# Performance work log

Measured on AMD Instinct MI355X. Metric: run time of the kernel, lower is better.

## Reference

```python
import jax, jax.numpy as jnp
import numpy as np

N_NODES = 100000
D = 128
N_EDGES = 800000


def setup_inputs() -> dict:
    key = jax.random.key(0)
    k_feat, k_src, k_dst, k_ws, k_wn = jax.random.split(key, 5)
    scale = 1.0 / np.sqrt(D)
    return {
        "features": jax.random.normal(k_feat, (N_NODES, D), jnp.float32),
        "src": jax.random.randint(k_src, (N_EDGES,), 0, N_NODES, jnp.int32),
        "dst": jax.random.randint(k_dst, (N_EDGES,), 0, N_NODES, jnp.int32),
        "gamma": jnp.ones((D,), jnp.float32),
        "beta": jnp.zeros((D,), jnp.float32),
        "W_self": jax.random.normal(k_ws, (D, D), jnp.float32) * scale,
        "W_neigh": jax.random.normal(k_wn, (D, D), jnp.float32) * scale,
        "b": jnp.zeros((D,), jnp.float32),
    }


def reference(features, src, dst, gamma, beta, W_self, W_neigh, b):
    n = features.shape[0]
    eps = 1e-5
    # BatchNorm1d (training mode: batch stats over the node dim, biased var)
    mean = jnp.mean(features, axis=0)
    var = jnp.mean(jnp.square(features - mean), axis=0)
    h = (features - mean) * jax.lax.rsqrt(var + eps) * gamma + beta  # [N, D]

    # SAGEConv 'mean': gather source feats along edges, mean-reduce per dst node
    msg = h[src]  # [E, D] irregular gather
    agg = jax.ops.segment_sum(msg, dst, num_segments=n)  # [N, D]
    deg = jax.ops.segment_sum(jnp.ones(src.shape, h.dtype), dst, num_segments=n)
    h_neigh = agg / jnp.maximum(deg, 1.0)[:, None]  # zero-degree nodes stay 0

    conv = h @ W_self + h_neigh @ W_neigh + b  # fc_self + fc_neigh + bias
    out = conv + h  # skip connection
    return jax.nn.gelu(out, approximate=False)
```

## Files before the change

### kernel.cpp

```cpp
#include <hip/hip_runtime.h>

#define DD 128
#define NPB_LOG 9
#define NPB 512
#define EPB 1024

typedef __attribute__((ext_vector_type(8))) short short8;
typedef __attribute__((ext_vector_type(4))) float f32x4;

__device__ inline unsigned short f2bf(float f) {
    unsigned u = __float_as_uint(f);
    unsigned r = u + 0x7fffu + ((u >> 16) & 1u);
    return (unsigned short)(r >> 16);
}
__device__ inline float bf2f(unsigned short s) {
    return __uint_as_float(((unsigned)s) << 16);
}

__global__ __launch_bounds__(256) void phase1_k(
    const float4* __restrict__ x, float* __restrict__ stats16, int n,
    const int* __restrict__ dst, int nE, int NCHUNK, int NBUCK,
    const float* __restrict__ Wself, const float* __restrict__ Wneigh,
    unsigned short* __restrict__ Bpre, int* __restrict__ cm) {
    int b = blockIdx.x, tid = threadIdx.x;
    __shared__ float ls[8][256];
    if (b < 16) {
        int q = b * 256 + tid;
        int l = q & 63;
        int kb = ((q >> 9) << 5) + ((l >> 4) << 3);
        int nn = (((q >> 6) & 7) << 4) + (l & 15);
        bool self = (kb < 128);
        const float* Wp = self ? (Wself + (size_t)kb * 128 + nn)
                               : (Wneigh + (size_t)(kb - 128) * 128 + nn);
        unsigned tmp[4];
#pragma unroll
        for (int j = 0; j < 4; ++j) {
            float v0 = Wp[(2 * j) * 128];
            float v1 = Wp[(2 * j + 1) * 128];
            if (self) {
                if (kb + 2 * j == nn) v0 += 1.0f;
                if (kb + 2 * j + 1 == nn) v1 += 1.0f;
            }
            tmp[j] = (unsigned)f2bf(v0) | ((unsigned)f2bf(v1) << 16);
        }
        uint4 w; w.x = tmp[0]; w.y = tmp[1]; w.z = tmp[2]; w.w = tmp[3];
        *(uint4*)(Bpre + (size_t)q * 8) = w;
    } else if (b < 16 + 1024) {
        int bb = b - 16;
        int c4 = tid & 31, sub = tid >> 5;
        float sx = 0.f, sy = 0.f, sz = 0.f, sw = 0.f;
        float qx = 0.f, qy = 0.f, qz = 0.f, qw = 0.f;
        for (int r = bb * 8 + sub; r < n; r += 1024 * 8) {
            float4 v = x[(size_t)r * 32 + c4];
            sx += v.x; sy += v.y; sz += v.z; sw += v.w;
            qx += v.x * v.x; qy += v.y * v.y; qz += v.z * v.z; qw += v.w * v.w;
        }
        ls[sub][c4 * 4 + 0] = sx; ls[sub][c4 * 4 + 1] = sy;
        ls[sub][c4 * 4 + 2] = sz; ls[sub][c4 * 4 + 3] = sw;
        ls[sub][128 + c4 * 4 + 0] = qx; ls[sub][128 + c4 * 4 + 1] = qy;
        ls[sub][128 + c4 * 4 + 2] = qz; ls[sub][128 + c4 * 4 + 3] = qw;
        __syncthreads();
        float t = 0.f;
#pragma unroll
        for (int k = 0; k < 8; ++k) t += ls[k][tid];
        atomicAdd(&stats16[(bb & 15) * 256 + tid], t);
    } else {
        int chunk = b - 1040;
        int* cnt = (int*)ls;
        for (int i = tid; i < NPB; i += 256) cnt[i] = 0;
        __syncthreads();
        int e0 = chunk * EPB;
#pragma unroll
        for (int j = 0; j < 4; ++j) {
            int e = e0 + j * 256 + tid;
            if (e < nE) atomicAdd(&cnt[dst[e] >> NPB_LOG], 1);
        }
        __syncthreads();
        for (int bk = tid; bk < NBUCK; bk += 256)
            cm[(size_t)bk * NCHUNK + chunk] = cnt[bk];
    }
}

__global__ __launch_bounds__(256) void scanA_k(
    const int* __restrict__ v_in, int* __restrict__ bsum, int n) {
    int b = blockIdx.x, t = threadIdx.x;
    int i0 = b * 1024 + t * 4;
    int4 v = {0, 0, 0, 0};
    if (i0 + 3 < n) v = *(const int4*)(v_in + i0);
    else {
        if (i0 < n) v.x = v_in[i0];
        if (i0 + 1 < n) v.y = v_in[i0 + 1];
        if (i0 + 2 < n) v.z = v_in[i0 + 2];
    }
    __shared__ int ls[256];
    ls[t] = v.x + v.y + v.z + v.w;
    __syncthreads();
#pragma unroll
    for (int off = 128; off > 0; off >>= 1) {
        if (t < off) ls[t] += ls[t + off];
        __syncthreads();
    }
    if (t == 0) bsum[b] = ls[0];
}

__global__ __launch_bounds__(256) void scanB_k(
    const int* __restrict__ bsum, int* __restrict__ bpref,
    int* __restrict__ total_out, int nb, int n) {
    __shared__ int ls[256];
    int t = threadIdx.x;
    ls[t] = (t < nb) ? bsum[t] : 0;
    __syncthreads();
#pragma unroll
    for (int off = 1; off < 256; off <<= 1) {
        int x = (t >= off) ? ls[t - off] : 0;
        __syncthreads();
        ls[t] += x;
        __syncthreads();
    }
    if (t < nb) bpref[t] = (t == 0) ? 0 : ls[t - 1];
    if (t == nb - 1) total_out[n] = ls[t];
}

__global__ __launch_bounds__(256) void scanC_k(
    const int* __restrict__ v_in, const int* __restrict__ bpref,
    int* __restrict__ o1, int* __restrict__ o2, int n) {
    int b = blockIdx.x, t = threadIdx.x;
    int i0 = b * 1024 + t * 4;
    int4 v = {0, 0, 0, 0};
    if (i0 + 3 < n) v = *(const int4*)(v_in + i0);
    else {
        if (i0 < n) v.x = v_in[i0];
        if (i0 + 1 < n) v.y = v_in[i0 + 1];
        if (i0 + 2 < n) v.z = v_in[i0 + 2];
    }
    int s = v.x + v.y + v.z + v.w;
    __shared__ int ls[256];
    ls[t] = s;
    __syncthreads();
#pragma unroll
    for (int off = 1; off < 256; off <<= 1) {
        int x = (t >= off) ? ls[t - off] : 0;
        __syncthreads();
        ls[t] += x;
        __syncthreads();
    }
    int run = bpref[b] + ((t == 0) ? 0 : ls[t - 1]);
    int4 o;
    o.x = run; o.y = run + v.x; o.z = o.y + v.y; o.w = o.z + v.z;
    if (i0 + 3 < n) {
        *(int4*)(o1 + i0) = o;
        *(int4*)(o2 + i0) = o;
    } else {
        if (i0 < n) { o1[i0] = o.x; o2[i0] = o.x; }
        if (i0 + 1 < n) { o1[i0 + 1] = o.y; o2[i0 + 1] = o.y; }
        if (i0 + 2 < n) { o1[i0 + 2] = o.z; o2[i0 + 2] = o.z; }
    }
}

__global__ __launch_bounds__(256) void phase2_k(
    const float4* __restrict__ x, const float* __restrict__ stats16,
    const float4* __restrict__ gamma, const float4* __restrict__ beta,
    uint2* __restrict__ hbuf, int n, float inv_n, int nbNorm,
    const int* __restrict__ src, const int* __restrict__ dst,
    const int* __restrict__ cmscan, unsigned* __restrict__ pairs,
    int nE, int NCHUNK, int NBUCK) {
    int b = blockIdx.x, tid = threadIdx.x;
    __shared__ int shr[512];
    if (b < nbNorm) {
        float* fs = (float*)shr;
        float a = 0.f;
#pragma unroll
        for (int sh = 0; sh < 16; ++sh) a += stats16[sh * 256 + tid];
        fs[tid] = a;
        __syncthreads();
        int c4 = tid & 31, sub = tid >> 5;
        int row = b * 8 + sub;
        float4 sm = ((const float4*)fs)[c4], sq = ((const float4*)fs)[32 + c4];
        float4 g = gamma[c4], bt = beta[c4];
        float mx = sm.x * inv_n, my = sm.y * inv_n, mz = sm.z * inv_n, mw = sm.w * inv_n;
        float vx = sq.x * inv_n - mx * mx, vy = sq.y * inv_n - my * my;
        float vz = sq.z * inv_n - mz * mz, vw = sq.w * inv_n - mw * mw;
        float scx = rsqrtf(vx + 1e-5f) * g.x, scy = rsqrtf(vy + 1e-5f) * g.y;
        float scz = rsqrtf(vz + 1e-5f) * g.z, scw = rsqrtf(vw + 1e-5f) * g.w;
        float shx = bt.x - mx * scx, shy = bt.y - my * scy;
        float shz = bt.z - mz * scz, shw = bt.w - mw * scw;
        if (row < n) {
            float4 v = x[(size_t)row * 32 + c4];
            float hx = v.x * scx + shx, hy = v.y * scy + shy;
            float hz = v.z * scz + shz, hw = v.w * scw + shw;
            uint2 o;
            o.x = (unsigned)f2bf(hx) | ((unsigned)f2bf(hy) << 16);
            o.y = (unsigned)f2bf(hz) | ((unsigned)f2bf(hw) << 16);
            hbuf[(size_t)row * 32 + c4] = o;
        }
    } else {
        int chunk = b - nbNorm;
        for (int i = tid; i < NBUCK; i += 256)
            shr[i] = cmscan[(size_t)i * NCHUNK + chunk];
        __syncthreads();
        int e0 = chunk * EPB;
#pragma unroll
        for (int j = 0; j < 4; ++j) {
            int e = e0 + j * 256 + tid;
            if (e < nE) {
                int d = dst[e];
                int p = atomicAdd(&shr[d >> NPB_LOG], 1);
                pairs[p] = ((unsigned)src[e] << NPB_LOG) | (unsigned)(d & (NPB - 1));
            }
        }
    }
}

__global__ __launch_bounds__(256) void sortC_k(
    const unsigned* __restrict__ pairs, const int* __restrict__ cmscan,
    int* __restrict__ offsets, int* __restrict__ csr,
    int n, int nE, int NCHUNK, int NBUCK) {
    int b = blockIdx.x, tid = threadIdx.x;
    int base0 = cmscan[(size_t)b * NCHUNK];
    int end = (b + 1 < NBUCK) ? cmscan[(size_t)(b + 1) * NCHUNK] : nE;
    __shared__ int cnt[NPB];
    __shared__ int cur[NPB];
    __shared__ int ps[256];
    for (int i = tid; i < NPB; i += 256) cnt[i] = 0;
    __syncthreads();
    for (int e = base0 + tid; e < end; e += 256)
        atomicAdd(&cnt[pairs[e] & (NPB - 1)], 1);
    __syncthreads();
    int c0 = cnt[2 * tid], c1 = cnt[2 * tid + 1];
    ps[tid] = c0 + c1;
    __syncthreads();
#pragma unroll
    for (int off = 1; off < 256; off <<= 1) {
        int v = (tid >= off) ? ps[tid - off] : 0;
        __syncthreads();
        ps[tid] += v;
        __syncthreads();
    }
    int ex = base0 + ((tid == 0) ? 0 : ps[tid - 1]);
    cur[2 * tid] = ex;
    cur[2 * tid + 1] = ex + c0;
    int node0 = b * NPB + 2 * tid;
    if (node0 < n) offsets[node0] = ex;
    if (node0 + 1 < n) offsets[node0 + 1] = ex + c0;
    if (b == NBUCK - 1 && tid == 0) offsets[n] = nE;
    __syncthreads();
    for (int e = base0 + tid; e < end; e += 256) {
        unsigned u = pairs[e];
        int p = atomicAdd(&cur[u & (NPB - 1)], 1);
        csr[p] = (int)(u >> NPB_LOG);
    }
}

__global__ __launch_bounds__(256) void pull_k(
    const int* __restrict__ offsets, const int* __restrict__ csr,
    const unsigned* __restrict__ h32, unsigned* __restrict__ hnw, int n) {
    int wid = (blockIdx.x * 256 + threadIdx.x) >> 6;
    int lane = threadIdx.x & 63;
    if (wid >= n) return;
    int b0 = offsets[wid], b1 = offsets[wid + 1];
    float a0 = 0.f, a1 = 0.f;
    int j = b0;
    for (; j + 8 <= b1; j += 8) {
        unsigned u[8];
#pragma unroll
        for (int q = 0; q < 8; ++q) u[q] = h32[(size_t)csr[j + q] * 64 + lane];
#pragma unroll
        for (int q = 0; q < 8; ++q) {
            a0 += bf2f((unsigned short)(u[q] & 0xffff));
            a1 += bf2f((unsigned short)(u[q] >> 16));
        }
    }
    for (; j + 2 <= b1; j += 2) {
        unsigned u0 = h32[(size_t)csr[j] * 64 + lane];
        unsigned u1 = h32[(size_t)csr[j + 1] * 64 + lane];
        a0 += bf2f((unsigned short)(u0 & 0xffff)) + bf2f((unsigned short)(u1 & 0xffff));
        a1 += bf2f((unsigned short)(u0 >> 16)) + bf2f((unsigned short)(u1 >> 16));
    }
    if (j < b1) {
        unsigned u0 = h32[(size_t)csr[j] * 64 + lane];
        a0 += bf2f((unsigned short)(u0 & 0xffff));
        a1 += bf2f((unsigned short)(u0 >> 16));
    }
    float rd = (b1 > b0) ? 1.0f / (float)(b1 - b0) : 0.0f;
    unsigned o = (unsigned)f2bf(a0 * rd) | ((unsigned)f2bf(a1 * rd) << 16);
    hnw[(size_t)wid * 64 + lane] = o;
}

__global__ __launch_bounds__(256, 4) void gemm_k(
    const unsigned short* __restrict__ h, const unsigned short* __restrict__ hn,
    const unsigned short* __restrict__ Bpre, const float* __restrict__ bias,
    float* __restrict__ out, int n) {
    __shared__ unsigned short Bsw[16384];
    int tid = threadIdx.x, wave = tid >> 6, lane = tid & 63;
    int H = blockIdx.x & 1, rb = blockIdx.x >> 1;
#pragma unroll
    for (int i = 0; i < 8; ++i) {
        int g = wave * 8 + i;
        int s = g >> 2, tt = g & 3;
        __builtin_amdgcn_global_load_lds(
            (const __attribute__((address_space(1))) void*)(
                Bpre + ((size_t)((s * 8 + H * 4 + tt) * 64) + lane) * 8),
            (__attribute__((address_space(3))) void*)(Bsw + (size_t)g * 512),
            16, 0, 0);
    }
    __syncthreads();

    int quad = lane >> 4, mrow = lane & 15;
    int r0 = rb * 128 + wave * 32;
    int rA0 = min(r0 + mrow, n - 1);
    int rA1 = min(r0 + 16 + mrow, n - 1);

    f32x4 zero = {0.0f, 0.0f, 0.0f, 0.0f};
    f32x4 acc[2][4];
#pragma unroll
    for (int m = 0; m < 2; ++m)
#pragma unroll
        for (int t = 0; t < 4; ++t) acc[m][t] = zero;

#pragma unroll
    for (int s = 0; s < 8; ++s) {
        int kb = s * 32 + quad * 8;
        short8 a0, a1;
        if (s < 4) {
            a0 = *(const short8*)(h + (size_t)rA0 * 128 + kb);
            a1 = *(const short8*)(h + (size_t)rA1 * 128 + kb);
        } else {
            int kk = kb - 128;
            a0 = *(const short8*)(hn + (size_t)rA0 * 128 + kk);
            a1 = *(const short8*)(hn + (size_t)rA1 * 128 + kk);
        }
#pragma unroll
        for (int tt = 0; tt < 4; ++tt) {
            short8 b = *(const short8*)(Bsw + ((size_t)(s * 4 + tt) * 64 + lane) * 8);
            acc[0][tt] = __builtin_amdgcn_mfma_f32_16x16x32_bf16(a0, b, acc[0][tt], 0, 0, 0);
            acc[1][tt] = __builtin_amdgcn_mfma_f32_16x16x32_bf16(a1, b, acc[1][tt], 0, 0, 0);
        }
    }

    float bi[4];
#pragma unroll
    for (int t = 0; t < 4; ++t) bi[t] = bias[H * 64 + t * 16 + mrow];
#pragma unroll
    for (int m = 0; m < 2; ++m) {
#pragma unroll
        for (int i = 0; i < 4; ++i) {
            int row = r0 + m * 16 + quad * 4 + i;
            if (row < n) {
#pragma unroll
                for (int t = 0; t < 4; ++t) {
                    int col = H * 64 + t * 16 + mrow;
                    float xv = acc[m][t][i] + bi[t];
                    float x2 = xv * xv;
                    float u = 0.7978845608f * xv * (1.0f + 0.044715f * x2);
                    float e = __expf(2.0f * u);
                    float th = 1.0f - 2.0f * __builtin_amdgcn_rcpf(e + 1.0f);
                    out[(size_t)row * 128 + col] = 0.5f * xv * (1.0f + th);
                }
            }
        }
    }
}

extern "C" void kernel_launch(void* const* d_in, const int* in_sizes, int n_in,
                              void* d_out, int out_size, void* d_ws, size_t ws_size,
                              hipStream_t stream) {
    const float* features = (const float*)d_in[0];
    const int* src = (const int*)d_in[1];
    const int* dst = (const int*)d_in[2];
    const float* gamma = (const float*)d_in[3];
    const float* beta = (const float*)d_in[4];
    const float* Wself = (const float*)d_in[5];
    const float* Wneigh = (const float*)d_in[6];
    const float* bias = (const float*)d_in[7];
    int n = in_sizes[0] / DD;
    int nE = in_sizes[1];
    int NCHUNK = (nE + EPB - 1) / EPB;
    int NBUCK = (n + NPB - 1) / NPB;
    int CM = NBUCK * NCHUNK;
    int tilesCM = (CM + 1023) / 1024;
    int nbNorm = (n + 7) / 8;

    auto align1k = [](size_t x) { return (x + 1023) & ~(size_t)1023; };
    char* ws = (char*)d_ws;
    size_t off = 0;
    float* stats16 = (float*)(ws + off);       off += 16384;
    int* cm       = (int*)(ws + off);          off += align1k((size_t)(CM + 1) * 4);
    int* cmscan   = (int*)(ws + off);          off += align1k((size_t)CM * 4);
    int* offsets  = (int*)(ws + off);          off += align1k((size_t)(n + 1) * 4);
    int* csr      = (int*)(ws + off);          off += align1k((size_t)nE * 4);
    unsigned* pairs = (unsigned*)(ws + off);   off += align1k((size_t)nE * 4);
    int* bsum     = (int*)(ws + off);          off += 1024;
    int* bpref    = (int*)(ws + off);          off += 1024;
    unsigned short* Bpre = (unsigned short*)(ws + off); off += 65536;
    unsigned short* hbuf = (unsigned short*)(ws + off); off += (size_t)n * 256;
    unsigned short* hnbuf = (unsigned short*)(ws + off); off += (size_t)n * 256;

    hipMemsetAsync(stats16, 0, 16384, stream);

    phase1_k<<<16 + 1024 + NCHUNK, 256, 0, stream>>>(
        (const float4*)features, stats16, n, dst, nE, NCHUNK, NBUCK,
        Wself, Wneigh, Bpre, cm);
    scanA_k<<<tilesCM, 256, 0, stream>>>(cm, bsum, CM);
    scanB_k<<<1, 256, 0, stream>>>(bsum, bpref, cm, tilesCM, CM);
    scanC_k<<<tilesCM, 256, 0, stream>>>(cm, bpref, cmscan, cmscan, CM);
    phase2_k<<<nbNorm + NCHUNK, 256, 0, stream>>>(
        (const float4*)features, stats16, (const float4*)gamma,
        (const float4*)beta, (uint2*)hbuf, n, 1.0f / (float)n, nbNorm,
        src, dst, cmscan, pairs, nE, NCHUNK, NBUCK);
    sortC_k<<<NBUCK, 256, 0, stream>>>(pairs, cmscan, offsets, csr, n, nE,
                                       NCHUNK, NBUCK);
    pull_k<<<(n * 64 + 255) / 256, 256, 0, stream>>>(
        offsets, csr, (const unsigned*)hbuf, (unsigned*)hnbuf, n);
    gemm_k<<<((n + 127) / 128) * 2, 256, 0, stream>>>(
        hbuf, hnbuf, Bpre, bias, (float*)d_out, n);
}
```

Measured before the change: 226.3 us.

## Gather neighbor features from an FP8 copy and retune bucket and chunk sizes

The normalize pass now also writes an FP8 (e4m3) copy of h alongside the bf16 copy. The neighbor-mean gather reads this copy, which halves the bytes fetched per random edge access in the bandwidth-bound pull stage. Separately, buckets shrink to 256 nodes and edge chunks grow to 2048 edges, which changes the counting-sort grid shapes and simplifies the per-bucket scan to one node per thread. The cost is an extra FP8 write pass and lower aggregation precision, which may push errors past tolerance.

```diff
diff --git a/kernel.cpp b/kernel.cpp
--- a/kernel.cpp
+++ b/kernel.cpp
@@ -1,12 +1,13 @@
 #include <hip/hip_runtime.h>
 
 #define DD 128
-#define NPB_LOG 9
-#define NPB 512
-#define EPB 1024
+#define NPB_LOG 8
+#define NPB 256
+#define EPB 2048
 
 typedef __attribute__((ext_vector_type(8))) short short8;
 typedef __attribute__((ext_vector_type(4))) float f32x4;
+typedef __attribute__((ext_vector_type(2))) float f32x2;
 
 __device__ inline unsigned short f2bf(float f) {
     unsigned u = __float_as_uint(f);
@@ -67,11 +68,11 @@
     } else {
         int chunk = b - 1040;
         int* cnt = (int*)ls;
-        for (int i = tid; i < NPB; i += 256) cnt[i] = 0;
+        for (int i = tid; i < NBUCK; i += 256) cnt[i] = 0;
         __syncthreads();
         int e0 = chunk * EPB;
 #pragma unroll
-        for (int j = 0; j < 4; ++j) {
+        for (int j = 0; j < 8; ++j) {
             int e = e0 + j * 256 + tid;
             if (e < nE) atomicAdd(&cnt[dst[e] >> NPB_LOG], 1);
         }
@@ -160,8 +161,8 @@
 __global__ __launch_bounds__(256) void phase2_k(
     const float4* __restrict__ x, const float* __restrict__ stats16,
     const float4* __restrict__ gamma, const float4* __restrict__ beta,
-    uint2* __restrict__ hbuf, int n, float inv_n, int nbNorm,
-    const int* __restrict__ src, const int* __restrict__ dst,
+    uint2* __restrict__ hbuf, unsigned* __restrict__ h8, int n, float inv_n,
+    int nbNorm, const int* __restrict__ src, const int* __restrict__ dst,
     const int* __restrict__ cmscan, unsigned* __restrict__ pairs,
     int nE, int NCHUNK, int NBUCK) {
     int b = blockIdx.x, tid = threadIdx.x;
@@ -192,6 +193,9 @@
             o.x = (unsigned)f2bf(hx) | ((unsigned)f2bf(hy) << 16);
             o.y = (unsigned)f2bf(hz) | ((unsigned)f2bf(hw) << 16);
             hbuf[(size_t)row * 32 + c4] = o;
+            int p8 = __builtin_amdgcn_cvt_pk_fp8_f32(hx, hy, 0, false);
+            p8 = __builtin_amdgcn_cvt_pk_fp8_f32(hz, hw, p8, true);
+            h8[(size_t)row * 32 + c4] = (unsigned)p8;
         }
     } else {
         int chunk = b - nbNorm;
@@ -200,7 +204,7 @@
         __syncthreads();
         int e0 = chunk * EPB;
 #pragma unroll
-        for (int j = 0; j < 4; ++j) {
+        for (int j = 0; j < 8; ++j) {
             int e = e0 + j * 256 + tid;
             if (e < nE) {
                 int d = dst[e];
@@ -220,14 +224,14 @@
     int end = (b + 1 < NBUCK) ? cmscan[(size_t)(b + 1) * NCHUNK] : nE;
     __shared__ int cnt[NPB];
     __shared__ int cur[NPB];
-    __shared__ int ps[256];
-    for (int i = tid; i < NPB; i += 256) cnt[i] = 0;
+    cnt[tid] = 0;
     __syncthreads();
     for (int e = base0 + tid; e < end; e += 256)
         atomicAdd(&cnt[pairs[e] & (NPB - 1)], 1);
     __syncthreads();
-    int c0 = cnt[2 * tid], c1 = cnt[2 * tid + 1];
-    ps[tid] = c0 + c1;
+    int c0 = cnt[tid];
+    __shared__ int ps[256];
+    ps[tid] = c0;
     __syncthreads();
 #pragma unroll
     for (int off = 1; off < 256; off <<= 1) {
@@ -236,12 +240,10 @@
         ps[tid] += v;
         __syncthreads();
     }
-    int ex = base0 + ((tid == 0) ? 0 : ps[tid - 1]);
-    cur[2 * tid] = ex;
-    cur[2 * tid + 1] = ex + c0;
-    int node0 = b * NPB + 2 * tid;
-    if (node0 < n) offsets[node0] = ex;
-    if (node0 + 1 < n) offsets[node0 + 1] = ex + c0;
+    int ex = base0 + ps[tid] - c0;
+    cur[tid] = ex;
+    int node = b * NPB + tid;
+    if (node < n) offsets[node] = ex;
     if (b == NBUCK - 1 && tid == 0) offsets[n] = nE;
     __syncthreads();
     for (int e = base0 + tid; e < end; e += 256) {
@@ -253,7 +255,7 @@
 
 __global__ __launch_bounds__(256) void pull_k(
     const int* __restrict__ offsets, const int* __restrict__ csr,
-    const unsigned* __restrict__ h32, unsigned* __restrict__ hnw, int n) {
+    const unsigned short* __restrict__ h8u, unsigned* __restrict__ hnw, int n) {
     int wid = (blockIdx.x * 256 + threadIdx.x) >> 6;
     int lane = threadIdx.x & 63;
     if (wid >= n) return;
@@ -261,25 +263,26 @@
     float a0 = 0.f, a1 = 0.f;
     int j = b0;
     for (; j + 8 <= b1; j += 8) {
-        unsigned u[8];
-#pragma unroll
-        for (int q = 0; q < 8; ++q) u[q] = h32[(size_t)csr[j + q] * 64 + lane];
+        unsigned short u[8];
+#pragma unroll
+        for (int q = 0; q < 8; ++q) u[q] = h8u[(size_t)csr[j + q] * 64 + lane];
 #pragma unroll
         for (int q = 0; q < 8; ++q) {
-            a0 += bf2f((unsigned short)(u[q] & 0xffff));
-            a1 += bf2f((unsigned short)(u[q] >> 16));
+            f32x2 fv = __builtin_amdgcn_cvt_pk_f32_fp8((unsigned)u[q], false);
+            a0 += fv.x; a1 += fv.y;
         }
     }
     for (; j + 2 <= b1; j += 2) {
-        unsigned u0 = h32[(size_t)csr[j] * 64 + lane];
-        unsigned u1 = h32[(size_t)csr[j + 1] * 64 + lane];
-        a0 += bf2f((unsigned short)(u0 & 0xffff)) + bf2f((unsigned short)(u1 & 0xffff));
-        a1 += bf2f((unsigned short)(u0 >> 16)) + bf2f((unsigned short)(u1 >> 16));
+        unsigned short u0 = h8u[(size_t)csr[j] * 64 + lane];
+        unsigned short u1 = h8u[(size_t)csr[j + 1] * 64 + lane];
+        f32x2 f0 = __builtin_amdgcn_cvt_pk_f32_fp8((unsigned)u0, false);
+        f32x2 f1 = __builtin_amdgcn_cvt_pk_f32_fp8((unsigned)u1, false);
+        a0 += f0.x + f1.x; a1 += f0.y + f1.y;
     }
     if (j < b1) {
-        unsigned u0 = h32[(size_t)csr[j] * 64 + lane];
-        a0 += bf2f((unsigned short)(u0 & 0xffff));
-        a1 += bf2f((unsigned short)(u0 >> 16));
+        unsigned short u0 = h8u[(size_t)csr[j] * 64 + lane];
+        f32x2 f0 = __builtin_amdgcn_cvt_pk_f32_fp8((unsigned)u0, false);
+        a0 += f0.x; a1 += f0.y;
     }
     float rd = (b1 > b0) ? 1.0f / (float)(b1 - b0) : 0.0f;
     unsigned o = (unsigned)f2bf(a0 * rd) | ((unsigned)f2bf(a1 * rd) << 16);
@@ -394,6 +397,7 @@
     unsigned short* Bpre = (unsigned short*)(ws + off); off += 65536;
     unsigned short* hbuf = (unsigned short*)(ws + off); off += (size_t)n * 256;
     unsigned short* hnbuf = (unsigned short*)(ws + off); off += (size_t)n * 256;
+    unsigned* h8 = (unsigned*)(ws + off);      off += (size_t)n * 128;
 
     hipMemsetAsync(stats16, 0, 16384, stream);
 
@@ -405,12 +409,12 @@
     scanC_k<<<tilesCM, 256, 0, stream>>>(cm, bpref, cmscan, cmscan, CM);
     phase2_k<<<nbNorm + NCHUNK, 256, 0, stream>>>(
         (const float4*)features, stats16, (const float4*)gamma,
-        (const float4*)beta, (uint2*)hbuf, n, 1.0f / (float)n, nbNorm,
+        (const float4*)beta, (uint2*)hbuf, h8, n, 1.0f / (float)n, nbNorm,
         src, dst, cmscan, pairs, nE, NCHUNK, NBUCK);
     sortC_k<<<NBUCK, 256, 0, stream>>>(pairs, cmscan, offsets, csr, n, nE,
                                        NCHUNK, NBUCK);
     pull_k<<<(n * 64 + 255) / 256, 256, 0, stream>>>(
-        offsets, csr, (const unsigned*)hbuf, (unsigned*)hnbuf, n);
+        offsets, csr, (const unsigned short*)h8, (unsigned*)hnbuf, n);
     gemm_k<<<((n + 127) / 128) * 2, 256, 0, stream>>>(
         hbuf, hnbuf, Bpre, bias, (float*)d_out, n);
 }
```

After: 225.2 us. No clear change (-0.5%).
